# Optimization experiments

Measured on AMD Instinct MI355X. Metric: run time of the kernel, lower is better.

The kernel has to match this reference:

```python
import jax, jax.numpy as jnp
import numpy as np
import math

N = 5000
H, W = 512, 512
CHUNK = 100                 # gaussians per scan step; CHUNK*H*W ~ 26M floats
ALPHA_THRESH = 1.0 / 255.0  # same skip threshold as the CUDA rasterizer
TWO_PI = 2.0 * math.pi


def setup_inputs() -> dict:
    key = jax.random.key(0)
    k1, k2, k3, k4 = jax.random.split(key, 4)
    return {
        "_xyz": jax.random.normal(k1, (N, 2), dtype=jnp.float32),
        "_scaling": jax.random.uniform(k2, (N, 2), dtype=jnp.float32),
        "_rotation": jax.random.uniform(k3, (N, 1), dtype=jnp.float32),
        "_features_dc": jax.random.uniform(k4, (N, 3), dtype=jnp.float32),
        "_opacity": jnp.ones((N, 1), dtype=jnp.float32),
    }


def _render(_xyz, _scaling, _rotation, _features_dc, _opacity):
    # --- parameter activations (GaussianImage_RS getters) ---
    means = jnp.tanh(_xyz)                          # [N,2] in (-1,1)
    scale = jnp.abs(_scaling + 0.5)                 # [N,2]  (bound = 0.5)
    theta = jax.nn.sigmoid(_rotation[:, 0]) * TWO_PI

    # --- project_gaussians_2d_scale_rot ---
    # ndc -> pixel centers
    cx = 0.5 * ((means[:, 0] + 1.0) * W - 1.0)      # [N]
    cy = 0.5 * ((means[:, 1] + 1.0) * H - 1.0)
    cth, sth = jnp.cos(theta), jnp.sin(theta)
    sx2 = scale[:, 0] * scale[:, 0]
    sy2 = scale[:, 1] * scale[:, 1]
    # cov2d = R S S^T R^T with R = [[c,-s],[s,c]]
    a = cth * cth * sx2 + sth * sth * sy2
    b = cth * sth * (sx2 - sy2)
    c = sth * sth * sx2 + cth * cth * sy2
    det = a * c - b * b
    valid = det > 0.0
    inv_det = jnp.where(valid, 1.0 / jnp.maximum(det, 1e-12), 0.0)
    A = c * inv_det                                  # conic xx
    B = -b * inv_det                                 # conic xy
    C = a * inv_det                                  # conic yy

    opac = _opacity[:, 0]                            # [N]
    cols = _features_dc                              # [N,3]

    ys, xs = jnp.meshgrid(jnp.arange(H, dtype=jnp.float32),
                          jnp.arange(W, dtype=jnp.float32), indexing="ij")

    # --- rasterize_gaussians_sum: out[p] = sum_i color_i * alpha_i(p) ---
    # scan over gaussian chunks to bound memory (CHUNK x H x W working set)
    def body(acc, g):
        gcx, gcy, gA, gB, gC, gop, gv, gcol = g
        dx = gcx[:, None, None] - xs[None]           # [c,H,W]
        dy = gcy[:, None, None] - ys[None]
        sigma = 0.5 * (gA[:, None, None] * dx * dx
                       + gC[:, None, None] * dy * dy) \
                + gB[:, None, None] * dx * dy
        alpha = gop[:, None, None] * jnp.exp(-sigma)
        alpha = jnp.where((sigma >= 0.0) & (alpha > ALPHA_THRESH)
                          & gv[:, None, None], alpha, 0.0)
        acc = acc + jnp.einsum("chw,ck->hwk", alpha, gcol)
        return acc, None

    def chunked(x):
        return x.reshape(N // CHUNK, CHUNK, *x.shape[1:])

    gauss = tuple(chunked(x) for x in (cx, cy, A, B, C, opac, valid, cols))
    img0 = jnp.zeros((H, W, 3), dtype=jnp.float32)
    img, _ = jax.lax.scan(body, img0, gauss)

    img = jnp.clip(img, 0.0, 1.0)
    # view(-1,H,W,3).permute(0,3,1,2)
    return img.reshape(1, H, W, 3).transpose(0, 3, 1, 2)


def reference(_xyz, _scaling, _rotation, _features_dc, _opacity):
    return _render(_xyz, _scaling, _rotation, _features_dc, _opacity)
```

## Files before the change

### kernel.cpp

```cpp
#include <hip/hip_runtime.h>
#include <math.h>

#define N_G       5000
#define HH        512
#define WW        512
#define TILE      16
#define TDIM      32
#define NTILES    (TDIM * TDIM)
#define ALPHA_TH  (1.0f / 255.0f)
#define TWO_PI_F  6.28318530717958647692f

__global__ __launch_bounds__(256) void k_prep(
    const float* __restrict__ xyz, const float* __restrict__ scal,
    const float* __restrict__ rot, const float* __restrict__ fdc,
    const float* __restrict__ opac,
    float4* __restrict__ rec, float4* __restrict__ cull)
{
    int i = blockIdx.x * blockDim.x + threadIdx.x;
    if (i >= N_G) return;

    float mx = tanhf(xyz[2 * i + 0]);
    float my = tanhf(xyz[2 * i + 1]);
    float sx = fabsf(scal[2 * i + 0] + 0.5f);
    float sy = fabsf(scal[2 * i + 1] + 0.5f);
    float th = (1.0f / (1.0f + expf(-rot[i]))) * TWO_PI_F;

    float cx = 0.5f * ((mx + 1.0f) * (float)WW - 1.0f);
    float cy = 0.5f * ((my + 1.0f) * (float)HH - 1.0f);
    float cth = cosf(th), sth = sinf(th);
    float sx2 = sx * sx, sy2 = sy * sy;
    float a = cth * cth * sx2 + sth * sth * sy2;
    float b = cth * sth * (sx2 - sy2);
    float c = sth * sth * sx2 + cth * cth * sy2;
    float det = a * c - b * b;
    bool valid = det > 0.0f;
    float inv_det = valid ? 1.0f / fmaxf(det, 1e-12f) : 0.0f;
    float A = c * inv_det, B = -b * inv_det, C = a * inv_det;
    float op = opac[i];

    float radius = 0.0f;
    if (valid && op > ALPHA_TH) {
        float tau  = logf(op * 255.0f);
        float mid  = 0.5f * (a + c);
        float rad  = sqrtf(fmaxf(0.0f, 0.25f * (a - c) * (a - c) + b * b));
        float lmax = mid + rad;
        radius = sqrtf(fmaxf(0.0f, 2.0f * tau * lmax)) * 1.0001f + 0.01f;
    }

    rec[3 * i + 0] = make_float4(cx, cy, A, B);
    rec[3 * i + 1] = make_float4(C, op, fdc[3 * i + 0], fdc[3 * i + 1]);
    rec[3 * i + 2] = make_float4(fdc[3 * i + 2], 0.0f, 0.0f, 0.0f);
    cull[i]        = make_float4(cx, cy, radius, 0.0f);
}

__global__ __launch_bounds__(256) void k_render(
    const float4* __restrict__ rec, const float4* __restrict__ cull,
    float* __restrict__ out)
{
    __shared__ int list[N_G];
    __shared__ int cnt;

    int t  = blockIdx.x;
    int tx = t & (TDIM - 1);
    int ty = t >> 5;
    int lx = threadIdx.x & (TILE - 1);
    int ly = threadIdx.x >> 4;
    int w  = tx * TILE + lx;
    int h  = ty * TILE + ly;
    float fx = (float)w, fy = (float)h;

    float x0 = (float)(tx * TILE), x1 = (float)(tx * TILE + TILE - 1);
    float y0 = (float)(ty * TILE), y1 = (float)(ty * TILE + TILE - 1);

    if (threadIdx.x == 0) cnt = 0;
    __syncthreads();

    for (int base = 0; base < N_G; base += 256) {
        int i = base + threadIdx.x;
        if (i < N_G) {
            float4 q = cull[i];
            float nx  = fminf(fmaxf(q.x, x0), x1);
            float ny  = fminf(fmaxf(q.y, y0), y1);
            float ddx = q.x - nx;
            float ddy = q.y - ny;
            if (ddx * ddx + ddy * ddy < q.z * q.z) {
                int p = atomicAdd(&cnt, 1);
                list[p] = i;
            }
        }
    }
    __syncthreads();
    int e = cnt;

    float r0 = 0.0f, r1 = 0.0f, r2 = 0.0f;
    for (int k = 0; k < e; ++k) {
        int gi = list[k];
        float4 pa = rec[3 * gi + 0];
        float4 pb = rec[3 * gi + 1];
        float4 pc = rec[3 * gi + 2];
        float dx = pa.x - fx;
        float dy = pa.y - fy;
        float sigma = 0.5f * (pa.z * dx * dx + pb.x * dy * dy) + pa.w * dx * dy;
        float alpha = pb.y * __expf(-sigma);
        bool pass = (sigma >= 0.0f) && (alpha > ALPHA_TH);
        float wg = pass ? alpha : 0.0f;
        r0 += wg * pb.z;
        r1 += wg * pb.w;
        r2 += wg * pc.x;
    }

    int pix = h * WW + w;
    out[0 * HH * WW + pix] = fminf(fmaxf(r0, 0.0f), 1.0f);
    out[1 * HH * WW + pix] = fminf(fmaxf(r1, 0.0f), 1.0f);
    out[2 * HH * WW + pix] = fminf(fmaxf(r2, 0.0f), 1.0f);
}

extern "C" void kernel_launch(void* const* d_in, const int* in_sizes, int n_in,
                              void* d_out, int out_size, void* d_ws, size_t ws_size,
                              hipStream_t stream) {
    const float* xyz  = (const float*)d_in[0];
    const float* scal = (const float*)d_in[1];
    const float* rot  = (const float*)d_in[2];
    const float* fdc  = (const float*)d_in[3];
    const float* opac = (const float*)d_in[4];
    float* out = (float*)d_out;

    float4* rec  = (float4*)d_ws;
    float4* cull = rec + 3 * N_G;

    k_prep<<<dim3((N_G + 255) / 256), dim3(256), 0, stream>>>(
        xyz, scal, rot, fdc, opac, rec, cull);
    k_render<<<dim3(NTILES), dim3(256), 0, stream>>>(rec, cull, out);
}
```

Measured before the change: 80.36 us.

## Fuse preprocessing into per-tile render with shared-memory gaussian records

Merges the prep and render kernels into one launch. Each tile block recomputes a conservative cull radius from the scales directly, then builds full conic records for only the surviving gaussians and stores them in shared memory, so the inner loop reads LDS instead of gathering from global memory. This removes one launch and the workspace round-trip, but every tile repeats tanh/log work for all 5000 gaussians. The per-tile list is also capped at 512 entries, so a tile with more overlapping gaussians would silently drop some.

```diff
diff --git a/kernel.cpp b/kernel.cpp
--- a/kernel.cpp
+++ b/kernel.cpp
@@ -7,58 +7,18 @@
 #define TILE      16
 #define TDIM      32
 #define NTILES    (TDIM * TDIM)
+#define CAP       512
 #define ALPHA_TH  (1.0f / 255.0f)
 #define TWO_PI_F  6.28318530717958647692f
 
-__global__ __launch_bounds__(256) void k_prep(
+__global__ __launch_bounds__(256) void k_fused(
     const float* __restrict__ xyz, const float* __restrict__ scal,
     const float* __restrict__ rot, const float* __restrict__ fdc,
-    const float* __restrict__ opac,
-    float4* __restrict__ rec, float4* __restrict__ cull)
+    const float* __restrict__ opac, float* __restrict__ out)
 {
-    int i = blockIdx.x * blockDim.x + threadIdx.x;
-    if (i >= N_G) return;
-
-    float mx = tanhf(xyz[2 * i + 0]);
-    float my = tanhf(xyz[2 * i + 1]);
-    float sx = fabsf(scal[2 * i + 0] + 0.5f);
-    float sy = fabsf(scal[2 * i + 1] + 0.5f);
-    float th = (1.0f / (1.0f + expf(-rot[i]))) * TWO_PI_F;
-
-    float cx = 0.5f * ((mx + 1.0f) * (float)WW - 1.0f);
-    float cy = 0.5f * ((my + 1.0f) * (float)HH - 1.0f);
-    float cth = cosf(th), sth = sinf(th);
-    float sx2 = sx * sx, sy2 = sy * sy;
-    float a = cth * cth * sx2 + sth * sth * sy2;
-    float b = cth * sth * (sx2 - sy2);
-    float c = sth * sth * sx2 + cth * cth * sy2;
-    float det = a * c - b * b;
-    bool valid = det > 0.0f;
-    float inv_det = valid ? 1.0f / fmaxf(det, 1e-12f) : 0.0f;
-    float A = c * inv_det, B = -b * inv_det, C = a * inv_det;
-    float op = opac[i];
-
-    float radius = 0.0f;
-    if (valid && op > ALPHA_TH) {
-        float tau  = logf(op * 255.0f);
-        float mid  = 0.5f * (a + c);
-        float rad  = sqrtf(fmaxf(0.0f, 0.25f * (a - c) * (a - c) + b * b));
-        float lmax = mid + rad;
-        radius = sqrtf(fmaxf(0.0f, 2.0f * tau * lmax)) * 1.0001f + 0.01f;
-    }
-
-    rec[3 * i + 0] = make_float4(cx, cy, A, B);
-    rec[3 * i + 1] = make_float4(C, op, fdc[3 * i + 0], fdc[3 * i + 1]);
-    rec[3 * i + 2] = make_float4(fdc[3 * i + 2], 0.0f, 0.0f, 0.0f);
-    cull[i]        = make_float4(cx, cy, radius, 0.0f);
-}
-
-__global__ __launch_bounds__(256) void k_render(
-    const float4* __restrict__ rec, const float4* __restrict__ cull,
-    float* __restrict__ out)
-{
-    __shared__ int list[N_G];
-    __shared__ int cnt;
+    __shared__ int    idx[CAP];
+    __shared__ float4 rec[CAP][3];
+    __shared__ int    cnt;
 
     int t  = blockIdx.x;
     int tx = t & (TDIM - 1);
@@ -69,35 +29,77 @@
     int h  = ty * TILE + ly;
     float fx = (float)w, fy = (float)h;
 
-    float x0 = (float)(tx * TILE), x1 = (float)(tx * TILE + TILE - 1);
-    float y0 = (float)(ty * TILE), y1 = (float)(ty * TILE + TILE - 1);
+    float bx0 = (float)(tx * TILE), bx1 = (float)(tx * TILE + TILE - 1);
+    float by0 = (float)(ty * TILE), by1 = (float)(ty * TILE + TILE - 1);
 
     if (threadIdx.x == 0) cnt = 0;
     __syncthreads();
 
+    const float2* xyz2  = (const float2*)xyz;
+    const float2* scal2 = (const float2*)scal;
     for (int base = 0; base < N_G; base += 256) {
         int i = base + threadIdx.x;
         if (i < N_G) {
-            float4 q = cull[i];
-            float nx  = fminf(fmaxf(q.x, x0), x1);
-            float ny  = fminf(fmaxf(q.y, y0), y1);
-            float ddx = q.x - nx;
-            float ddy = q.y - ny;
-            if (ddx * ddx + ddy * ddy < q.z * q.z) {
-                int p = atomicAdd(&cnt, 1);
-                list[p] = i;
+            float2 p  = xyz2[i];
+            float2 s2 = scal2[i];
+            float  op = opac[i];
+            float cx = 0.5f * ((tanhf(p.x) + 1.0f) * (float)WW - 1.0f);
+            float cy = 0.5f * ((tanhf(p.y) + 1.0f) * (float)HH - 1.0f);
+            float sx = fabsf(s2.x + 0.5f);
+            float sy = fabsf(s2.y + 0.5f);
+            float lmax = fmaxf(sx * sx, sy * sy);
+            bool  keep = false;
+            if (op > ALPHA_TH && lmax > 0.0f) {
+                float tau = logf(op * 255.0f);
+                float r   = sqrtf(fmaxf(0.0f, 2.0f * tau * lmax)) + 0.1f;
+                float nx  = fminf(fmaxf(cx, bx0), bx1);
+                float ny  = fminf(fmaxf(cy, by0), by1);
+                float ddx = cx - nx;
+                float ddy = cy - ny;
+                keep = (ddx * ddx + ddy * ddy) < r * r;
+            }
+            if (keep) {
+                int pos = atomicAdd(&cnt, 1);
+                if (pos < CAP) idx[pos] = i;
             }
         }
     }
     __syncthreads();
-    int e = cnt;
+    int e = min(cnt, CAP);
+
+    for (int k = threadIdx.x; k < e; k += 256) {
+        int i = idx[k];
+        float2 p  = xyz2[i];
+        float2 s2 = scal2[i];
+        float mx = tanhf(p.x);
+        float my = tanhf(p.y);
+        float sx = fabsf(s2.x + 0.5f);
+        float sy = fabsf(s2.y + 0.5f);
+        float th = (1.0f / (1.0f + expf(-rot[i]))) * TWO_PI_F;
+        float cx = 0.5f * ((mx + 1.0f) * (float)WW - 1.0f);
+        float cy = 0.5f * ((my + 1.0f) * (float)HH - 1.0f);
+        float cth, sth;
+        __sincosf(th, &sth, &cth);
+        float sx2 = sx * sx, sy2 = sy * sy;
+        float a = cth * cth * sx2 + sth * sth * sy2;
+        float b = cth * sth * (sx2 - sy2);
+        float c = sth * sth * sx2 + cth * cth * sy2;
+        float det = a * c - b * b;
+        bool valid = det > 0.0f;
+        float inv_det = valid ? 1.0f / fmaxf(det, 1e-12f) : 0.0f;
+        float A = c * inv_det, B = -b * inv_det, C = a * inv_det;
+        float op = valid ? opac[i] : 0.0f;
+        rec[k][0] = make_float4(cx, cy, A, B);
+        rec[k][1] = make_float4(C, op, fdc[3 * i + 0], fdc[3 * i + 1]);
+        rec[k][2] = make_float4(fdc[3 * i + 2], 0.0f, 0.0f, 0.0f);
+    }
+    __syncthreads();
 
     float r0 = 0.0f, r1 = 0.0f, r2 = 0.0f;
     for (int k = 0; k < e; ++k) {
-        int gi = list[k];
-        float4 pa = rec[3 * gi + 0];
-        float4 pb = rec[3 * gi + 1];
-        float4 pc = rec[3 * gi + 2];
+        float4 pa = rec[k][0];
+        float4 pb = rec[k][1];
+        float4 pc = rec[k][2];
         float dx = pa.x - fx;
         float dy = pa.y - fy;
         float sigma = 0.5f * (pa.z * dx * dx + pb.x * dy * dy) + pa.w * dx * dy;
@@ -125,10 +127,6 @@
     const float* opac = (const float*)d_in[4];
     float* out = (float*)d_out;
 
-    float4* rec  = (float4*)d_ws;
-    float4* cull = rec + 3 * N_G;
-
-    k_prep<<<dim3((N_G + 255) / 256), dim3(256), 0, stream>>>(
-        xyz, scal, rot, fdc, opac, rec, cull);
-    k_render<<<dim3(NTILES), dim3(256), 0, stream>>>(rec, cull, out);
+    k_fused<<<dim3(NTILES), dim3(256), 0, stream>>>(
+        xyz, scal, rot, fdc, opac, out);
 }
```

After: 80.67 us. No clear change (+0.4%).
